# Optimization experiments

Measured on AMD Instinct MI355X. Metric: run time of the kernel, lower is better.

The kernel has to match this reference:

```python
import jax, jax.numpy as jnp
import numpy as np

B, SV, SA, D, H, L, F = 1, 2048, 512, 1024, 16, 2, 4096
DH = D // H
S = SV + SA


def layer_norm(x):
    mu = jnp.mean(x, axis=-1, keepdims=True)
    var = jnp.var(x, axis=-1, keepdims=True)
    return (x - mu) * jax.lax.rsqrt(var + 1e-6)


def rms_norm(x, g):
    return x * jax.lax.rsqrt(jnp.mean(x * x, axis=-1, keepdims=True) + 1e-6) * g


def rope(x, theta):
    # x: [B,S,H*DH], theta: [S, DH//2] angles; complex-pair rotation as in rope_apply
    b, s, _ = x.shape
    x4 = x.reshape(b, s, H, DH)
    xe, xo = x4[..., 0::2], x4[..., 1::2]
    c = jnp.cos(theta)[None, :, None, :]
    sn = jnp.sin(theta)[None, :, None, :]
    re = xe * c - xo * sn
    im = xe * sn + xo * c
    return jnp.stack([re, im], axis=-1).reshape(b, s, H * DH)


def setup_inputs() -> dict:
    key = jax.random.key(0)
    ks = jax.random.split(key, 20)
    w = 0.02
    inp = {
        'video_tokens': jax.random.normal(ks[0], (B, SV, D), jnp.float32),
        'action_tokens': jax.random.normal(ks[1], (B, SA, D), jnp.float32),
        'video_freqs': jax.random.uniform(ks[2], (SV, DH // 2), jnp.float32) * 6.28,
        'action_freqs': jax.random.uniform(ks[3], (SA, DH // 2), jnp.float32) * 6.28,
        'video_t_mod': jax.random.normal(ks[4], (B, 6, D), jnp.float32),
        'action_t_mod': jax.random.normal(ks[5], (B, 6, D), jnp.float32),
        'Wq': jax.random.normal(ks[6], (2, L, D, D), jnp.float32) * w,
        'Wk': jax.random.normal(ks[7], (2, L, D, D), jnp.float32) * w,
        'Wv': jax.random.normal(ks[8], (2, L, D, D), jnp.float32) * w,
        'Wo': jax.random.normal(ks[9], (2, L, D, D), jnp.float32) * w,
        'bq': jnp.zeros((2, L, D), jnp.float32),
        'bk': jnp.zeros((2, L, D), jnp.float32),
        'bv': jnp.zeros((2, L, D), jnp.float32),
        'bo': jnp.zeros((2, L, D), jnp.float32),
        'gq': jnp.ones((2, L, D), jnp.float32),
        'gk': jnp.ones((2, L, D), jnp.float32),
        'mod': jax.random.normal(ks[10], (2, L, 6, D), jnp.float32) * 0.02,
        'W1': jax.random.normal(ks[11], (2, L, D, F), jnp.float32) * w,
        'b1': jnp.zeros((2, L, F), jnp.float32),
        'W2': jax.random.normal(ks[12], (2, L, F, D), jnp.float32) * w,
        'b2': jnp.zeros((2, L, D), jnp.float32),
    }
    # Mixed-modality ctx_mask: video bidirectional; action attends video + causal over action
    m = np.zeros((S, S), dtype=bool)
    m[:SV, :SV] = True
    m[SV:, :SV] = True
    m[SV:, SV:] = np.tril(np.ones((SA, SA), dtype=bool))
    inp['attention_mask'] = jnp.asarray(m)
    return inp


def _mot_forward(video_tokens, action_tokens, video_freqs, action_freqs,
                 video_t_mod, action_t_mod, Wq, Wk, Wv, Wo, bq, bk, bv, bo,
                 gq, gk, mod, W1, b1, W2, b2, attention_mask):
    xs = [video_tokens, action_tokens]
    thetas = [video_freqs, action_freqs]
    tmods = [video_t_mod, action_t_mod]
    scale = 1.0 / jnp.sqrt(jnp.asarray(DH, xs[0].dtype))
    for l in range(L):
        qs, kss, vs, posts = [], [], [], []
        for e in range(2):
            m6 = mod[e, l][None] + tmods[e]  # [B,6,D]
            sh_msa, sc_msa, g_msa, sh_mlp, sc_mlp, g_mlp = (
                m6[:, i:i + 1, :] for i in range(6))
            a = layer_norm(xs[e]) * (1.0 + sc_msa) + sh_msa
            q = rope(rms_norm(a @ Wq[e, l] + bq[e, l], gq[e, l]), thetas[e])
            k = rope(rms_norm(a @ Wk[e, l] + bk[e, l], gk[e, l]), thetas[e])
            v = a @ Wv[e, l] + bv[e, l]
            qs.append(q); kss.append(k); vs.append(v)
            posts.append((g_msa, sh_mlp, sc_mlp, g_mlp))
        qc = jnp.concatenate(qs, axis=1).reshape(B, S, H, DH)
        kc = jnp.concatenate(kss, axis=1).reshape(B, S, H, DH)
        vc = jnp.concatenate(vs, axis=1).reshape(B, S, H, DH)
        scores = jnp.einsum('bqhd,bkhd->bhqk', qc, kc) * scale
        scores = jnp.where(attention_mask[None, None], scores, -1e9)
        p = jax.nn.softmax(scores, axis=-1)
        o = jnp.einsum('bhqk,bkhd->bqhd', p, vc).reshape(B, S, H * DH)
        outs = [o[:, :SV], o[:, SV:]]
        for e in range(2):
            g_msa, sh_mlp, sc_mlp, g_mlp = posts[e]
            x = xs[e] + g_msa * (outs[e] @ Wo[e, l] + bo[e, l])
            mi = layer_norm(x) * (1.0 + sc_mlp) + sh_mlp
            h = jax.nn.gelu(mi @ W1[e, l] + b1[e, l], approximate=True) @ W2[e, l] + b2[e, l]
            xs[e] = x + g_mlp * h
    return jnp.concatenate(xs, axis=1)  # [B, SV+SA, D]


def reference(video_tokens, action_tokens, video_freqs, action_freqs,
              video_t_mod, action_t_mod, Wq, Wk, Wv, Wo, bq, bk, bv, bo,
              gq, gk, mod, W1, b1, W2, b2, attention_mask):
    return _mot_forward(video_tokens, action_tokens, video_freqs, action_freqs,
                        video_t_mod, action_t_mod, Wq, Wk, Wv, Wo, bq, bk, bv, bo,
                        gq, gk, mod, W1, b1, W2, b2, attention_mask)
```

## Files before the change

### kernel.cpp

```cpp
#include <hip/hip_runtime.h>
#include <hip/hip_bf16.h>

#define BF16 __hip_bfloat16
typedef short bf16x8 __attribute__((ext_vector_type(8)));
typedef float f32x4  __attribute__((ext_vector_type(4)));
typedef unsigned int u32;

#define MFMA16(a, b, c) __builtin_amdgcn_mfma_f32_16x16x32_bf16(a, b, c, 0, 0, 0)


__device__ __forceinline__ void async16(const void* g, void* l) {
  __builtin_amdgcn_global_load_lds(
      (const __attribute__((address_space(1))) u32*)g,
      (__attribute__((address_space(3))) u32*)l, 16, 0, 0);
}

__device__ __forceinline__ u32 pkbf(float a, float b) {
  union { BF16 h; unsigned short s; } ua, ub;
  ua.h = __float2bfloat16(a); ub.h = __float2bfloat16(b);
  return (u32)ua.s | ((u32)ub.s << 16);
}

__global__ __launch_bounds__(256) void wtrans(const float* __restrict__ W,
                                              BF16* __restrict__ WT, int K, int N,
                                              size_t outZ) {
  __shared__ float t[32][33];
  const float* Wm = W + (size_t)K * N * blockIdx.z;
  BF16* Tm = WT + outZ * blockIdx.z;
  int n0 = blockIdx.x * 32, k0 = blockIdx.y * 32;
  int tx = threadIdx.x & 31, ty = threadIdx.x >> 5;
#pragma unroll
  for (int i = 0; i < 4; i++)
    t[ty + 8 * i][tx] = Wm[(size_t)(k0 + ty + 8 * i) * N + n0 + tx];
  __syncthreads();
#pragma unroll
  for (int i = 0; i < 4; i++)
    Tm[(size_t)(n0 + ty + 8 * i) * K + k0 + tx] = __float2bfloat16(t[tx][ty + 8 * i]);
}

__global__ __launch_bounds__(256) void packb(const float* __restrict__ bq,
                                             const float* __restrict__ bk,
                                             const float* __restrict__ bv,
                                             float* __restrict__ bqkv) {
  int i = blockIdx.x * 256 + threadIdx.x;
  int s = i / 3072, c = i - s * 3072;
  float v = (c < 1024) ? bq[s * 1024 + c]
          : (c < 2048) ? bk[s * 1024 + c - 1024]
                       : bv[s * 1024 + c - 2048];
  bqkv[i] = v;
}

__global__ __launch_bounds__(256) void ln_mod(const float* __restrict__ x,
                                              BF16* __restrict__ out,
                                              const float* __restrict__ mod,
                                              const float* __restrict__ tmv,
                                              const float* __restrict__ tma,
                                              int l, int ish, int isc) {
  int r = blockIdx.x;
  int e = (r >= 2048) ? 1 : 0;
  const float* tm = e ? tma : tmv;
  const float* mo = mod + (size_t)((e * 2 + l) * 6) * 1024;
  float4 v = ((const float4*)(x + (size_t)r * 1024))[threadIdx.x];
  float s = v.x + v.y + v.z + v.w;
  float s2 = v.x * v.x + v.y * v.y + v.z * v.z + v.w * v.w;
#pragma unroll
  for (int off = 32; off >= 1; off >>= 1) {
    s += __shfl_down(s, off);
    s2 += __shfl_down(s2, off);
  }
  __shared__ float red[8];
  int lane = threadIdx.x & 63, w = threadIdx.x >> 6;
  if (lane == 0) { red[w] = s; red[4 + w] = s2; }
  __syncthreads();
  s = red[0] + red[1] + red[2] + red[3];
  s2 = red[4] + red[5] + red[6] + red[7];
  float mu = s * (1.f / 1024.f);
  float var = s2 * (1.f / 1024.f) - mu * mu;
  float inv = rsqrtf(var + 1e-6f);
  int c = threadIdx.x * 4;
  BF16* o = out + (size_t)r * 1024 + c;
  float xv[4] = {v.x, v.y, v.z, v.w};
#pragma unroll
  for (int k = 0; k < 4; k++) {
    float sc = mo[isc * 1024 + c + k] + tm[isc * 1024 + c + k];
    float sh = mo[ish * 1024 + c + k] + tm[ish * 1024 + c + k];
    o[k] = __float2bfloat16((xv[k] - mu) * inv * (1.f + sc) + sh);
  }
}

__global__ __launch_bounds__(256) void qk_post(const float* __restrict__ qkv,
                                               const float* __restrict__ gq,
                                               const float* __restrict__ gk,
                                               BF16* __restrict__ Qb, BF16* __restrict__ Kb,
                                               const float* __restrict__ vfreq,
                                               const float* __restrict__ afreq, int l) {
  int r = blockIdx.x;
  int which = blockIdx.y;
  const float* src = qkv + (size_t)r * 3072 + which * 1024;
  int e = (r >= 2048) ? 1 : 0;
  const float* g = (which ? gk : gq) + (size_t)(e * 2 + l) * 1024;
  BF16* dst = which ? Kb : Qb;
  const float* fr = e ? (afreq + (size_t)(r - 2048) * 32) : (vfreq + (size_t)r * 32);
  float4 v = ((const float4*)src)[threadIdx.x];
  float s2 = v.x * v.x + v.y * v.y + v.z * v.z + v.w * v.w;
#pragma unroll
  for (int off = 32; off >= 1; off >>= 1) s2 += __shfl_down(s2, off);
  __shared__ float red[4];
  int lane = threadIdx.x & 63, w = threadIdx.x >> 6;
  if (lane == 0) red[w] = s2;
  __syncthreads();
  s2 = red[0] + red[1] + red[2] + red[3];
  float inv = rsqrtf(s2 * (1.f / 1024.f) + 1e-6f);
  if (which == 0) inv *= 0.125f * 1.44269504f;
  int c = threadIdx.x * 4;
  float xe0 = v.x * inv * g[c], xo0 = v.y * inv * g[c + 1];
  float xe1 = v.z * inv * g[c + 2], xo1 = v.w * inv * g[c + 3];
  int p0 = (c & 63) >> 1;
  float c0, s0, c1, s1;
  __sincosf(fr[p0], &s0, &c0);
  __sincosf(fr[p0 + 1], &s1, &c1);
  int h = c >> 6;
  size_t o = ((size_t)h * 2560 + r) * 64 + (c & 63);
  dst[o + 0] = __float2bfloat16(xe0 * c0 - xo0 * s0);
  dst[o + 1] = __float2bfloat16(xe0 * s0 + xo0 * c0);
  dst[o + 2] = __float2bfloat16(xe1 * c1 - xo1 * s1);
  dst[o + 3] = __float2bfloat16(xe1 * s1 + xo1 * c1);
}

__global__ __launch_bounds__(256) void vpost(const float* __restrict__ qkv,
                                             BF16* __restrict__ VT) {
  __shared__ float t[32][33];
  int r0 = blockIdx.x * 32, c0 = blockIdx.y * 32;
  int tx = threadIdx.x & 31, ty = threadIdx.x >> 5;
#pragma unroll
  for (int i = 0; i < 4; i++)
    t[ty + 8 * i][tx] = qkv[(size_t)(r0 + ty + 8 * i) * 3072 + 2048 + c0 + tx];
  __syncthreads();
#pragma unroll
  for (int i = 0; i < 4; i++)
    VT[(size_t)(c0 + ty + 8 * i) * 2560 + r0 + tx] = __float2bfloat16(t[tx][ty + 8 * i]);
}

template <int EPI, int KS>
__global__ __launch_bounds__(256) void gemm2(const BF16* __restrict__ A,
                                             const BF16* __restrict__ Bw, size_t Bestride,
                                             const float* __restrict__ bias, int biasE,
                                             void* __restrict__ out, float* __restrict__ part,
                                             int N, int K) {
  __shared__ BF16 As[128 * 64];
  __shared__ BF16 Bs[128 * 64];
  int flat = blockIdx.x + blockIdx.y * gridDim.x;
  int xcd = flat & 7, slot = flat >> 3;
  int bx = slot % gridDim.x;
  int by = (slot / gridDim.x) * 8 + xcd;
  int m0 = bx * 128, n0 = by * 128;
  int e = (m0 >= 2048);
  const BF16* Ab = A + (size_t)m0 * K;
  const BF16* Bb = Bw + (e ? Bestride : 0) + (size_t)n0 * K;
  int kz0 = blockIdx.z * (K / KS), kz1 = kz0 + K / KS;
  int tid = threadIdx.x, lane = tid & 63, w = tid >> 6;
  int wr = w & 1, wc = w >> 1;
  int m15 = lane & 15, q4 = lane >> 4;
  int L[4], rS[4], cS[4];
#pragma unroll
  for (int i = 0; i < 4; i++) {
    L[i] = w * 256 + i * 64 + lane;
    rS[i] = L[i] >> 3;
    cS[i] = (L[i] & 7) ^ (rS[i] & 7);
  }
  f32x4 acc[4][4] = {};
  for (int k0 = kz0; k0 < kz1; k0 += 64) {
    __syncthreads();
#pragma unroll
    for (int i = 0; i < 4; i++) {
      async16(Ab + (size_t)rS[i] * K + k0 + cS[i] * 8, &As[L[i] * 8]);
      async16(Bb + (size_t)rS[i] * K + k0 + cS[i] * 8, &Bs[L[i] * 8]);
    }
    __syncthreads();
#pragma unroll
    for (int kk = 0; kk < 2; kk++) {
      int pos = ((kk * 4 + q4) ^ (m15 & 7)) * 8;
      bf16x8 af[4], bv[4];
#pragma unroll
      for (int i = 0; i < 4; i++) af[i] = *(const bf16x8*)&As[(wr * 64 + i * 16 + m15) * 64 + pos];
#pragma unroll
      for (int j = 0; j < 4; j++) bv[j] = *(const bf16x8*)&Bs[(wc * 64 + j * 16 + m15) * 64 + pos];
#pragma unroll
      for (int i = 0; i < 4; i++)
#pragma unroll
        for (int j = 0; j < 4; j++)
          acc[i][j] = MFMA16(af[i], bv[j], acc[i][j]);
    }
  }
#pragma unroll
  for (int i = 0; i < 4; i++) {
    int row = m0 + wr * 64 + 16 * i + q4 * 4;
#pragma unroll
    for (int j = 0; j < 4; j++) {
      int col = n0 + wc * 64 + 16 * j + m15;
      float b = (EPI == 3) ? 0.f : bias[e * biasE + col];
#pragma unroll
      for (int rg = 0; rg < 4; rg++) {
        float v = acc[i][j][rg] + b;
        size_t idx = (size_t)(row + rg) * N + col;
        if (EPI == 0) {
          ((float*)out)[idx] = v;
        } else if (EPI == 1) {
          float u = 0.7978845608f * (v + 0.044715f * v * v * v);
          ((BF16*)out)[idx] = __float2bfloat16(0.5f * v * (1.f + tanhf(u)));
        } else {
          part[(size_t)blockIdx.z * 2560 * N + idx] = v;
        }
      }
    }
  }
}

template <int KS>
__global__ __launch_bounds__(256) void combine(const float* __restrict__ part,
                                               const float* __restrict__ biasL,
                                               const float* __restrict__ modp, int gi, int l,
                                               const float* __restrict__ tmv,
                                               const float* __restrict__ tma,
                                               const float* __restrict__ xin,
                                               float* __restrict__ xout) {
  int r = blockIdx.x, e = (r >= 2048) ? 1 : 0;
  int c = threadIdx.x * 4;
  float4 s = {0.f, 0.f, 0.f, 0.f};
#pragma unroll
  for (int z = 0; z < KS; z++) {
    float4 p = *(const float4*)&part[((size_t)z * 2560 + r) * 1024 + c];
    s.x += p.x; s.y += p.y; s.z += p.z; s.w += p.w;
  }
  float4 b = *(const float4*)&biasL[e * 2048 + c];
  const float* tm = e ? tma : tmv;
  float4 gm = *(const float4*)&modp[(size_t)((e * 2 + l) * 6 + gi) * 1024 + c];
  float4 gt = *(const float4*)&tm[gi * 1024 + c];
  float4 xi = *(const float4*)&xin[(size_t)r * 1024 + c];
  float4 o;
  o.x = xi.x + (gm.x + gt.x) * (s.x + b.x);
  o.y = xi.y + (gm.y + gt.y) * (s.y + b.y);
  o.z = xi.z + (gm.z + gt.z) * (s.z + b.z);
  o.w = xi.w + (gm.w + gt.w) * (s.w + b.w);
  *(float4*)&xout[(size_t)r * 1024 + c] = o;
}

__global__ __launch_bounds__(256) void flash4(const BF16* __restrict__ Qb,
                                              const BF16* __restrict__ Kb,
                                              const BF16* __restrict__ VT,
                                              float* __restrict__ Op,
                                              float* __restrict__ ml) {
  const int S = 2560;
  __shared__ BF16 Ks[2][64 * 64];
  __shared__ BF16 Vs[2][64 * 64];
  __shared__ BF16 Ps[4][16 * 64];
  int tid = threadIdx.x, lane = tid & 63, w = tid >> 6;
  int h = blockIdx.y, q0 = blockIdx.x * 64, kz = blockIdx.z;
  int m15 = lane & 15, q4 = lane >> 4;
  int actq = (q0 >= 2048);
  int nt = actq ? ((q0 >> 6) + 1) : 32;
  int tb = kz ? (nt >> 1) : 0;
  int te = kz ? nt : (nt >> 1);
  const BF16* qrow = Qb + ((size_t)h * S + q0 + w * 16 + m15) * 64;
  bf16x8 qf0 = *(const bf16x8*)(qrow + q4 * 8);
  bf16x8 qf1 = *(const bf16x8*)(qrow + 32 + q4 * 8);
  const BF16* kbase = Kb + (size_t)h * S * 64;
  const BF16* vbase = VT + (size_t)h * 64 * S;
  int L0 = w * 128 + lane, L1 = L0 + 64;
  int r0 = L0 >> 3, c0 = (L0 & 7) ^ (r0 & 7);
  int r1 = L1 >> 3, c1 = (L1 & 7) ^ (r1 & 7);
  {
    const BF16* kg = kbase + (size_t)tb * 64 * 64;
    const BF16* vg = vbase + (size_t)tb * 64;
    async16(kg + (size_t)r0 * 64 + c0 * 8, &Ks[0][L0 * 8]);
    async16(kg + (size_t)r1 * 64 + c1 * 8, &Ks[0][L1 * 8]);
    async16(vg + (size_t)r0 * S + c0 * 8, &Vs[0][L0 * 8]);
    async16(vg + (size_t)r1 * S + c1 * 8, &Vs[0][L1 * 8]);
  }
  f32x4 oa[4] = {};
  float m_i = -1e30f, l_i = 0.f;
  int colq = q0 + w * 16 + m15;
  char* Pw = (char*)&Ps[w][0];
  int prow = m15 * 128;
  int pswz = (m15 & 7) << 4;
  int x0 = (q4 ^ (m15 & 7)) * 8, x1 = ((4 + q4) ^ (m15 & 7)) * 8;
  __syncthreads();
  for (int t = tb; t < te; t++) {
    int cur = (t - tb) & 1;
    if (t + 1 < te) {
      int nb = cur ^ 1;
      const BF16* kg = kbase + (size_t)(t + 1) * 64 * 64;
      const BF16* vg = vbase + (size_t)(t + 1) * 64;
      async16(kg + (size_t)r0 * 64 + c0 * 8, &Ks[nb][L0 * 8]);
      async16(kg + (size_t)r1 * 64 + c1 * 8, &Ks[nb][L1 * 8]);
      async16(vg + (size_t)r0 * S + c0 * 8, &Vs[nb][L0 * 8]);
      async16(vg + (size_t)r1 * S + c1 * 8, &Vs[nb][L1 * 8]);
    }
    f32x4 st[4];
#pragma unroll
    for (int jt = 0; jt < 4; jt++) {
      int row = (jt * 16 + m15) * 64;
      bf16x8 kf0 = *(const bf16x8*)&Ks[cur][row + x0];
      bf16x8 kf1 = *(const bf16x8*)&Ks[cur][row + x1];
      f32x4 zz = {};
      zz = MFMA16(kf0, qf0, zz);
      st[jt] = MFMA16(kf1, qf1, zz);
    }
    float mx = -1e30f;
    if (actq && t == nt - 1) {
#pragma unroll
      for (int jt = 0; jt < 4; jt++)
#pragma unroll
        for (int rg = 0; rg < 4; rg++) {
          int rowkv = t * 64 + jt * 16 + q4 * 4 + rg;
          if (rowkv > colq) st[jt][rg] = -1e30f;
          mx = fmaxf(mx, st[jt][rg]);
        }
    } else {
#pragma unroll
      for (int jt = 0; jt < 4; jt++) {
        mx = fmaxf(fmaxf(mx, st[jt][0]), st[jt][1]);
        mx = fmaxf(fmaxf(mx, st[jt][2]), st[jt][3]);
      }
    }
    mx = fmaxf(mx, __shfl_xor(mx, 16));
    mx = fmaxf(mx, __shfl_xor(mx, 32));
    if (!__all(mx <= m_i + 8.f)) {
      float mn = fmaxf(m_i, mx);
      float al = exp2f(m_i - mn);
      m_i = mn;
      l_i *= al;
      float alr[4];
#pragma unroll
      for (int rg = 0; rg < 4; rg++) alr[rg] = __shfl(al, q4 * 4 + rg);
#pragma unroll
      for (int dt = 0; dt < 4; dt++)
#pragma unroll
        for (int rg = 0; rg < 4; rg++) oa[dt][rg] *= alr[rg];
    }
    float rs = 0.f;
#pragma unroll
    for (int jt = 0; jt < 4; jt++) {
      float p0 = exp2f(st[jt][0] - m_i), p1 = exp2f(st[jt][1] - m_i);
      float p2 = exp2f(st[jt][2] - m_i), p3 = exp2f(st[jt][3] - m_i);
      rs += (p0 + p1) + (p2 + p3);
      uint2 pr = {pkbf(p0, p1), pkbf(p2, p3)};
      *(uint2*)(Pw + prow + ((jt * 32 + q4 * 8) ^ pswz)) = pr;
    }
    rs += __shfl_xor(rs, 16);
    rs += __shfl_xor(rs, 32);
    l_i += rs;
    bf16x8 pf0 = *(const bf16x8*)(Pw + prow + ((q4 * 16) ^ pswz));
    bf16x8 pf1 = *(const bf16x8*)(Pw + prow + ((64 + q4 * 16) ^ pswz));
#pragma unroll
    for (int dt = 0; dt < 4; dt++) {
      int vr = (dt * 16 + m15) * 64;
      bf16x8 vf0 = *(const bf16x8*)&Vs[cur][vr + x0];
      bf16x8 vf1 = *(const bf16x8*)&Vs[cur][vr + x1];
      oa[dt] = MFMA16(pf0, vf0, oa[dt]);
      oa[dt] = MFMA16(pf1, vf1, oa[dt]);
    }
    __syncthreads();
  }
  size_t ob = (((size_t)kz * 16 + h) * 40 + blockIdx.x) * 4096;
#pragma unroll
  for (int dt = 0; dt < 4; dt++)
#pragma unroll
    for (int rg = 0; rg < 4; rg++)
      Op[ob + (size_t)(w * 16 + q4 * 4 + rg) * 64 + dt * 16 + m15] = oa[dt][rg];
  if (q4 == 0) {
    float* mp = ml + (((size_t)kz * 16 + h) * 40 + blockIdx.x) * 128;
    mp[w * 16 + m15] = m_i;
    mp[64 + w * 16 + m15] = l_i;
  }
}

__global__ __launch_bounds__(256) void fcomb(const float* __restrict__ Op,
                                             const float* __restrict__ ml,
                                             BF16* __restrict__ O) {
  int qt = blockIdx.x, h = blockIdx.y;
  int q = threadIdx.x >> 2;
  int d0 = (threadIdx.x & 3) * 16;
  size_t tile = (size_t)h * 40 + qt;
  const size_t zO = (size_t)16 * 40 * 4096;
  const size_t zm = (size_t)16 * 40 * 128;
  size_t base = tile * 4096 + (size_t)q * 64 + d0;
  size_t mb = tile * 128 + q;
  float m0 = ml[mb], l0 = ml[mb + 64];
  float m1 = ml[zm + mb], l1 = ml[zm + mb + 64];
  float M = fmaxf(m0, m1);
  float a = exp2f(m0 - M), b = exp2f(m1 - M);
  float r = 1.f / (a * l0 + b * l1);
  a *= r; b *= r;
  BF16* orow = O + (size_t)(qt * 64 + q) * 1024 + h * 64 + d0;
#pragma unroll
  for (int i = 0; i < 4; i++) {
    float4 x0 = *(const float4*)&Op[base + i * 4];
    float4 x1 = *(const float4*)&Op[zO + base + i * 4];
    uint2 pr = {pkbf(a * x0.x + b * x1.x, a * x0.y + b * x1.y),
                pkbf(a * x0.z + b * x1.z, a * x0.w + b * x1.w)};
    *(uint2*)(orow + i * 4) = pr;
  }
}

extern "C" void kernel_launch(void* const* d_in, const int* in_sizes, int n_in,
                              void* d_out, int out_size, void* d_ws, size_t ws_size,
                              hipStream_t stream) {
  (void)in_sizes; (void)n_in; (void)out_size; (void)ws_size;
  const float* vid  = (const float*)d_in[0];
  const float* act  = (const float*)d_in[1];
  const float* vfr  = (const float*)d_in[2];
  const float* afr  = (const float*)d_in[3];
  const float* tmv  = (const float*)d_in[4];
  const float* tma  = (const float*)d_in[5];
  const float* Wq   = (const float*)d_in[6];
  const float* Wk   = (const float*)d_in[7];
  const float* Wv   = (const float*)d_in[8];
  const float* Wo   = (const float*)d_in[9];
  const float* bq   = (const float*)d_in[10];
  const float* bk   = (const float*)d_in[11];
  const float* bv   = (const float*)d_in[12];
  const float* bo   = (const float*)d_in[13];
  const float* gq   = (const float*)d_in[14];
  const float* gk   = (const float*)d_in[15];
  const float* modp = (const float*)d_in[16];
  const float* W1   = (const float*)d_in[17];
  const float* b1   = (const float*)d_in[18];
  const float* W2   = (const float*)d_in[19];
  const float* b2   = (const float*)d_in[20];

  char* p = (char*)d_ws;
  auto carve = [&](size_t bytes) {
    char* r = p;
    p += (bytes + 255) & ~(size_t)255;
    return r;
  };
  BF16* WqkvT = (BF16*)carve(4ull * 3072 * 1024 * 2);
  BF16* WoT   = (BF16*)carve(4ull * 1024 * 1024 * 2);
  BF16* W1T   = (BF16*)carve(4ull * 4096 * 1024 * 2);
  BF16* W2T   = (BF16*)carve(4ull * 1024 * 4096 * 2);
  float* bqkv = (float*)carve(4ull * 3072 * 4);
  float* x    = (float*)carve(2560ull * 1024 * 4);
  BF16* abf   = (BF16*)carve(2560ull * 1024 * 2);
  float* qkv  = (float*)carve(2560ull * 3072 * 4);
  BF16* Qb    = (BF16*)carve(2560ull * 1024 * 2);
  BF16* Kb    = (BF16*)carve(2560ull * 1024 * 2);
  float* part = qkv;
  float* Opar = qkv;
  float* mlb  = qkv + 2ull * 16 * 40 * 4096;
  BF16* VTb   = (BF16*)carve(2560ull * 1024 * 2);
  BF16* Obf   = (BF16*)carve(2560ull * 1024 * 2);
  BF16* mibf  = (BF16*)carve(2560ull * 1024 * 2);
  BF16* hbf   = (BF16*)carve(2560ull * 4096 * 2);

  hipMemcpyAsync(x, vid, 2048ull * 1024 * 4, hipMemcpyDeviceToDevice, stream);
  hipMemcpyAsync(x + 2048ull * 1024, act, 512ull * 1024 * 4, hipMemcpyDeviceToDevice, stream);

  const size_t S3 = 3072ull * 1024;
  wtrans<<<dim3(32, 32, 4), 256, 0, stream>>>(Wq, WqkvT, 1024, 1024, S3);
  wtrans<<<dim3(32, 32, 4), 256, 0, stream>>>(Wk, WqkvT + 1024ull * 1024, 1024, 1024, S3);
  wtrans<<<dim3(32, 32, 4), 256, 0, stream>>>(Wv, WqkvT + 2048ull * 1024, 1024, 1024, S3);
  wtrans<<<dim3(32, 32, 4), 256, 0, stream>>>(Wo, WoT, 1024, 1024, 1024ull * 1024);
  wtrans<<<dim3(128, 32, 4), 256, 0, stream>>>(W1, W1T, 1024, 4096, 4096ull * 1024);
  wtrans<<<dim3(32, 128, 4), 256, 0, stream>>>(W2, W2T, 4096, 1024, 1024ull * 4096);
  packb<<<48, 256, 0, stream>>>(bq, bk, bv, bqkv);

  for (int l = 0; l < 2; l++) {
    ln_mod<<<2560, 256, 0, stream>>>(x, abf, modp, tmv, tma, l, 0, 1);
    gemm2<0, 1><<<dim3(20, 24, 1), 256, 0, stream>>>(
        abf, WqkvT + (size_t)l * S3, 2 * S3, bqkv + l * 3072, 6144, qkv, nullptr, 3072, 1024);
    qk_post<<<dim3(2560, 2), 256, 0, stream>>>(qkv, gq, gk, Qb, Kb, vfr, afr, l);
    vpost<<<dim3(80, 32), 256, 0, stream>>>(qkv, VTb);
    flash4<<<dim3(40, 16, 2), 256, 0, stream>>>(Qb, Kb, VTb, Opar, mlb);
    fcomb<<<dim3(40, 16), 256, 0, stream>>>(Opar, mlb, Obf);
    gemm2<3, 2><<<dim3(20, 8, 2), 256, 0, stream>>>(
        Obf, WoT + (size_t)l * 1024 * 1024, 2ull * 1024 * 1024, nullptr, 0, nullptr, part,
        1024, 1024);
    combine<2><<<2560, 256, 0, stream>>>(part, bo + l * 1024, modp, 2, l, tmv, tma, x, x);
    ln_mod<<<2560, 256, 0, stream>>>(x, mibf, modp, tmv, tma, l, 3, 4);
    gemm2<1, 1><<<dim3(20, 32, 1), 256, 0, stream>>>(
        mibf, W1T + (size_t)l * 4096 * 1024, 2ull * 4096 * 1024, b1 + l * 4096, 8192, hbf,
        nullptr, 4096, 1024);
    gemm2<3, 4><<<dim3(20, 8, 4), 256, 0, stream>>>(
        hbf, W2T + (size_t)l * 4096 * 1024, 2ull * 4096 * 1024, nullptr, 0, nullptr, part,
        1024, 4096);
    combine<4><<<2560, 256, 0, stream>>>(part, b2 + l * 1024, modp, 5, l, tmv, tma, x,
                                         (l == 1) ? (float*)d_out : x);
  }
}
```

Baseline: 757.7 us.

## Split flash attention KV range four ways, defer row reductions, cheaper GELU

The flash attention kernel now splits each query tile's KV range into four chunks instead of two. This doubles the block count to improve occupancy and tail balance. Partial outputs go to the qkv buffer and the idle hbf buffer, and a four-way combine kernel merges them. Per-tile cross-lane max and row-sum shuffles now run only on rescale or once at the end, and s_setprio is raised around the MFMA sections. The GELU epilogue swaps tanhf for an exp2/rcp sigmoid form, at the cost of extra partial-output traffic and slightly different rounding.

```diff
diff --git a/kernel.cpp b/kernel.cpp
--- a/kernel.cpp
+++ b/kernel.cpp
@@ -206,8 +206,9 @@
         if (EPI == 0) {
           ((float*)out)[idx] = v;
         } else if (EPI == 1) {
-          float u = 0.7978845608f * (v + 0.044715f * v * v * v);
-          ((BF16*)out)[idx] = __float2bfloat16(0.5f * v * (1.f + tanhf(u)));
+          float u = v * (0.7978845608f + 0.0356774081f * v * v);
+          float d = 1.f + exp2f(-2.8853900818f * u);
+          ((BF16*)out)[idx] = __float2bfloat16(v * __builtin_amdgcn_rcpf(d));
         } else {
           part[(size_t)blockIdx.z * 2560 * N + idx] = v;
         }
@@ -245,12 +246,15 @@
   *(float4*)&xout[(size_t)r * 1024 + c] = o;
 }
 
-__global__ __launch_bounds__(256) void flash4(const BF16* __restrict__ Qb,
+__global__ __launch_bounds__(256) void flash5(const BF16* __restrict__ Qb,
                                               const BF16* __restrict__ Kb,
                                               const BF16* __restrict__ VT,
-                                              float* __restrict__ Op,
+                                              float* __restrict__ OpA,
+                                              float* __restrict__ OpB,
                                               float* __restrict__ ml) {
   const int S = 2560;
+  const size_t ZO = 16ull * 40 * 4096;
+  const size_t ZM = 16ull * 40 * 128;
   __shared__ BF16 Ks[2][64 * 64];
   __shared__ BF16 Vs[2][64 * 64];
   __shared__ BF16 Ps[4][16 * 64];
@@ -259,8 +263,7 @@
   int m15 = lane & 15, q4 = lane >> 4;
   int actq = (q0 >= 2048);
   int nt = actq ? ((q0 >> 6) + 1) : 32;
-  int tb = kz ? (nt >> 1) : 0;
-  int te = kz ? nt : (nt >> 1);
+  int tb = (kz * nt) >> 2, te = ((kz + 1) * nt) >> 2;
   const BF16* qrow = Qb + ((size_t)h * S + q0 + w * 16 + m15) * 64;
   bf16x8 qf0 = *(const bf16x8*)(qrow + q4 * 8);
   bf16x8 qf1 = *(const bf16x8*)(qrow + 32 + q4 * 8);
@@ -297,6 +300,7 @@
       async16(vg + (size_t)r1 * S + c1 * 8, &Vs[nb][L1 * 8]);
     }
     f32x4 st[4];
+    __builtin_amdgcn_s_setprio(1);
 #pragma unroll
     for (int jt = 0; jt < 4; jt++) {
       int row = (jt * 16 + m15) * 64;
@@ -306,6 +310,7 @@
       zz = MFMA16(kf0, qf0, zz);
       st[jt] = MFMA16(kf1, qf1, zz);
     }
+    __builtin_amdgcn_s_setprio(0);
     float mx = -1e30f;
     if (actq && t == nt - 1) {
 #pragma unroll
@@ -323,10 +328,10 @@
         mx = fmaxf(fmaxf(mx, st[jt][2]), st[jt][3]);
       }
     }
-    mx = fmaxf(mx, __shfl_xor(mx, 16));
-    mx = fmaxf(mx, __shfl_xor(mx, 32));
     if (!__all(mx <= m_i + 8.f)) {
-      float mn = fmaxf(m_i, mx);
+      float m2 = fmaxf(mx, __shfl_xor(mx, 16));
+      m2 = fmaxf(m2, __shfl_xor(m2, 32));
+      float mn = fmaxf(m_i, m2);
       float al = exp2f(m_i - mn);
       m_i = mn;
       l_i *= al;
@@ -347,11 +352,10 @@
       uint2 pr = {pkbf(p0, p1), pkbf(p2, p3)};
       *(uint2*)(Pw + prow + ((jt * 32 + q4 * 8) ^ pswz)) = pr;
     }
-    rs += __shfl_xor(rs, 16);
-    rs += __shfl_xor(rs, 32);
     l_i += rs;
     bf16x8 pf0 = *(const bf16x8*)(Pw + prow + ((q4 * 16) ^ pswz));
     bf16x8 pf1 = *(const bf16x8*)(Pw + prow + ((64 + q4 * 16) ^ pswz));
+    __builtin_amdgcn_s_setprio(1);
 #pragma unroll
     for (int dt = 0; dt < 4; dt++) {
       int vr = (dt * 16 + m15) * 64;
@@ -360,45 +364,70 @@
       oa[dt] = MFMA16(pf0, vf0, oa[dt]);
       oa[dt] = MFMA16(pf1, vf1, oa[dt]);
     }
+    __builtin_amdgcn_s_setprio(0);
     __syncthreads();
   }
-  size_t ob = (((size_t)kz * 16 + h) * 40 + blockIdx.x) * 4096;
+  l_i += __shfl_xor(l_i, 16);
+  l_i += __shfl_xor(l_i, 32);
+  float* Op = (kz < 2) ? (OpA + (size_t)kz * ZO) : (OpB + (size_t)(kz - 2) * ZO);
+  size_t ob = ((size_t)h * 40 + blockIdx.x) * 4096;
 #pragma unroll
   for (int dt = 0; dt < 4; dt++)
 #pragma unroll
     for (int rg = 0; rg < 4; rg++)
       Op[ob + (size_t)(w * 16 + q4 * 4 + rg) * 64 + dt * 16 + m15] = oa[dt][rg];
   if (q4 == 0) {
-    float* mp = ml + (((size_t)kz * 16 + h) * 40 + blockIdx.x) * 128;
+    float* mp = ml + (size_t)kz * ZM + ((size_t)h * 40 + blockIdx.x) * 128;
     mp[w * 16 + m15] = m_i;
     mp[64 + w * 16 + m15] = l_i;
   }
 }
 
-__global__ __launch_bounds__(256) void fcomb(const float* __restrict__ Op,
-                                             const float* __restrict__ ml,
-                                             BF16* __restrict__ O) {
+__global__ __launch_bounds__(256) void fcomb4(const float* __restrict__ OpA,
+                                              const float* __restrict__ OpB,
+                                              const float* __restrict__ ml,
+                                              BF16* __restrict__ O) {
   int qt = blockIdx.x, h = blockIdx.y;
   int q = threadIdx.x >> 2;
   int d0 = (threadIdx.x & 3) * 16;
+  const size_t ZO = 16ull * 40 * 4096;
+  const size_t ZM = 16ull * 40 * 128;
   size_t tile = (size_t)h * 40 + qt;
-  const size_t zO = (size_t)16 * 40 * 4096;
-  const size_t zm = (size_t)16 * 40 * 128;
   size_t base = tile * 4096 + (size_t)q * 64 + d0;
   size_t mb = tile * 128 + q;
-  float m0 = ml[mb], l0 = ml[mb + 64];
-  float m1 = ml[zm + mb], l1 = ml[zm + mb + 64];
-  float M = fmaxf(m0, m1);
-  float a = exp2f(m0 - M), b = exp2f(m1 - M);
-  float r = 1.f / (a * l0 + b * l1);
-  a *= r; b *= r;
+  float m[4], lv[4];
+#pragma unroll
+  for (int z = 0; z < 4; z++) {
+    m[z] = ml[z * ZM + mb];
+    lv[z] = ml[z * ZM + mb + 64];
+  }
+  float M = fmaxf(fmaxf(m[0], m[1]), fmaxf(m[2], m[3]));
+  float wz[4];
+  float den = 0.f;
+#pragma unroll
+  for (int z = 0; z < 4; z++) {
+    wz[z] = exp2f(m[z] - M);
+    den += wz[z] * lv[z];
+  }
+  float r = 1.f / den;
+#pragma unroll
+  for (int z = 0; z < 4; z++) wz[z] *= r;
+  const float* P0 = OpA + base;
+  const float* P1 = OpA + ZO + base;
+  const float* P2 = OpB + base;
+  const float* P3 = OpB + ZO + base;
   BF16* orow = O + (size_t)(qt * 64 + q) * 1024 + h * 64 + d0;
 #pragma unroll
   for (int i = 0; i < 4; i++) {
-    float4 x0 = *(const float4*)&Op[base + i * 4];
-    float4 x1 = *(const float4*)&Op[zO + base + i * 4];
-    uint2 pr = {pkbf(a * x0.x + b * x1.x, a * x0.y + b * x1.y),
-                pkbf(a * x0.z + b * x1.z, a * x0.w + b * x1.w)};
+    float4 a0 = *(const float4*)&P0[i * 4];
+    float4 a1 = *(const float4*)&P1[i * 4];
+    float4 a2 = *(const float4*)&P2[i * 4];
+    float4 a3 = *(const float4*)&P3[i * 4];
+    float vx = wz[0] * a0.x + wz[1] * a1.x + wz[2] * a2.x + wz[3] * a3.x;
+    float vy = wz[0] * a0.y + wz[1] * a1.y + wz[2] * a2.y + wz[3] * a3.y;
+    float vzv = wz[0] * a0.z + wz[1] * a1.z + wz[2] * a2.z + wz[3] * a3.z;
+    float vw = wz[0] * a0.w + wz[1] * a1.w + wz[2] * a2.w + wz[3] * a3.w;
+    uint2 pr = {pkbf(vx, vy), pkbf(vzv, vw)};
     *(uint2*)(orow + i * 4) = pr;
   }
 }
@@ -446,12 +475,14 @@
   BF16* Qb    = (BF16*)carve(2560ull * 1024 * 2);
   BF16* Kb    = (BF16*)carve(2560ull * 1024 * 2);
   float* part = qkv;
-  float* Opar = qkv;
-  float* mlb  = qkv + 2ull * 16 * 40 * 4096;
+  const size_t ZO = 16ull * 40 * 4096;
+  float* OpA = qkv;
+  float* mlb = qkv + 2ull * ZO;
   BF16* VTb   = (BF16*)carve(2560ull * 1024 * 2);
   BF16* Obf   = (BF16*)carve(2560ull * 1024 * 2);
   BF16* mibf  = (BF16*)carve(2560ull * 1024 * 2);
   BF16* hbf   = (BF16*)carve(2560ull * 4096 * 2);
+  float* OpB = (float*)hbf;
 
   hipMemcpyAsync(x, vid, 2048ull * 1024 * 4, hipMemcpyDeviceToDevice, stream);
   hipMemcpyAsync(x + 2048ull * 1024, act, 512ull * 1024 * 4, hipMemcpyDeviceToDevice, stream);
@@ -471,8 +502,8 @@
         abf, WqkvT + (size_t)l * S3, 2 * S3, bqkv + l * 3072, 6144, qkv, nullptr, 3072, 1024);
     qk_post<<<dim3(2560, 2), 256, 0, stream>>>(qkv, gq, gk, Qb, Kb, vfr, afr, l);
     vpost<<<dim3(80, 32), 256, 0, stream>>>(qkv, VTb);
-    flash4<<<dim3(40, 16, 2), 256, 0, stream>>>(Qb, Kb, VTb, Opar, mlb);
-    fcomb<<<dim3(40, 16), 256, 0, stream>>>(Opar, mlb, Obf);
+    flash5<<<dim3(40, 16, 4), 256, 0, stream>>>(Qb, Kb, VTb, OpA, OpB, mlb);
+    fcomb4<<<dim3(40, 16), 256, 0, stream>>>(OpA, OpB, mlb, Obf);
     gemm2<3, 2><<<dim3(20, 8, 2), 256, 0, stream>>>(
         Obf, WoT + (size_t)l * 1024 * 1024, 2ull * 1024 * 1024, nullptr, 0, nullptr, part,
         1024, 1024);
```

New measurement: 766.9 us. No clear change (+1.2%).
